# Kernel optimization log

Hardware: AMD Instinct MI355X
Metric: run time of the kernel (lower is better)

## Reference

```python
import jax, jax.numpy as jnp
import numpy as np

HEADS = 16
DIM_HEAD = 64

def setup_inputs() -> dict:
    key = jax.random.key(0)
    k1, k2, k3 = jax.random.split(key, 3)
    B, F, N, DIM = 4, 16, 196, 1024
    ntok = 1 + F * N  # cls + frames*patches
    x = jax.random.normal(k1, (B, ntok, DIM), dtype=jnp.float32)
    w_qkv = jax.random.normal(k2, (DIM, 3 * HEADS * DIM_HEAD), dtype=jnp.float32) * (DIM ** -0.5)
    w_out = jax.random.normal(k3, (HEADS * DIM_HEAD, DIM), dtype=jnp.float32) * ((HEADS * DIM_HEAD) ** -0.5)
    return {"x": x, "w_qkv": w_qkv, "w_out": w_out, "f": F}

def _attn(q, k, v):
    # q: [b, i, d], k/v: [b, j, d]
    sim = jnp.einsum('bid,bjd->bij', q, k)
    a = jax.nn.softmax(sim, axis=-1)
    return jnp.einsum('bij,bjd->bid', a, v)

def reference(x, w_qkv, w_out, f):
    B, ntok, dim = x.shape
    h, dh = HEADS, DIM_HEAD
    n = (ntok - 1) // f  # patches per frame
    scale = dh ** -0.5

    qkv = x @ w_qkv  # [B, ntok, 3*h*dh]
    q, k, v = jnp.split(qkv, 3, axis=-1)
    # 'b n (h d) -> (b h) n d'
    def split_heads(t):
        return t.reshape(B, ntok, h, dh).transpose(0, 2, 1, 3).reshape(B * h, ntok, dh)
    q, k, v = split_heads(q) * scale, split_heads(k), split_heads(v)

    cls_q, q_ = q[:, :1], q[:, 1:]
    cls_k, k_ = k[:, :1], k[:, 1:]
    cls_v, v_ = v[:, :1], v[:, 1:]

    # cls token attends to everything
    cls_out = _attn(cls_q, k, v)  # [(b h), 1, d]

    # axial rearrange: '(b h) (f n) d -> (b h f) n d' (spatial attention)
    def to_axial(t):
        return t.reshape(B * h, f, n, dh).reshape(B * h * f, n, dh)
    q_, k_, v_ = map(to_axial, (q_, k_, v_))

    # broadcast cls kv to each frame: 'b () d -> (b r) () d', r = f
    cls_k_r = jnp.repeat(cls_k, f, axis=0)
    cls_v_r = jnp.repeat(cls_v, f, axis=0)
    k_ = jnp.concatenate((cls_k_r, k_), axis=1)  # [(b h f), 1+n, d]
    v_ = jnp.concatenate((cls_v_r, v_), axis=1)

    out = _attn(q_, k_, v_)  # [(b h f), n, d]
    # back: '(b h f) n d -> (b h) (f n) d'
    out = out.reshape(B * h, f * n, dh)
    out = jnp.concatenate((cls_out, out), axis=1)  # [(b h), ntok, d]
    # '(b h) n d -> b n (h d)'
    out = out.reshape(B, h, ntok, dh).transpose(0, 2, 1, 3).reshape(B, ntok, h * dh)
    return out @ w_out
```

## Files before the change

### kernel.cpp

```cpp
#include <hip/hip_runtime.h>
#include <stdint.h>

typedef unsigned short u16;
typedef unsigned int u32;
typedef __attribute__((ext_vector_type(4))) float f32x4;
typedef __attribute__((ext_vector_type(4))) float float4v;
typedef __attribute__((ext_vector_type(8))) short short8;
typedef __attribute__((ext_vector_type(4))) u32 u32x4;
typedef __attribute__((ext_vector_type(4))) u16 u16x4;
typedef __attribute__((ext_vector_type(8))) u16 u16x8;

#define DEV static __device__ __forceinline__

#define NTOK 3137
#define MROWS 12548
#define NHEAD 16
#define DH 64
#define NKT 16

DEV float bf2f(u16 h){ u32 u = ((u32)h)<<16; float f; __builtin_memcpy(&f,&u,4); return f; }
DEV u16 f2bf(float f){ u32 u; __builtin_memcpy(&u,&f,4); u32 r = u + 0x7FFFu + ((u>>16)&1u); return (u16)(r>>16); }

DEV void gl_lds16(const u16* g, u16* l){
  __builtin_amdgcn_global_load_lds((const __attribute__((address_space(1))) void*)g,
                                   (__attribute__((address_space(3))) void*)l, 16, 0, 0);
}

#define BARRIER()  asm volatile("s_barrier" ::: "memory")
#define WAIT_LGKM0() asm volatile("s_waitcnt lgkmcnt(0)" ::: "memory")
#define WAIT_VM(n)  asm volatile("s_waitcnt vmcnt(" #n ")" ::: "memory")

__global__ __launch_bounds__(256) void cast_bf16_kernel(const float* __restrict__ in,
                                                        u16* __restrict__ out, int n4){
  int i = blockIdx.x*256 + threadIdx.x;
  int stride = gridDim.x*256;
  for(; i < n4; i += stride){
    float4v v = *(const float4v*)(in + (size_t)i*4);
    u16x4 o;
    for(int e=0;e<4;++e) o[e] = f2bf(v[e]);
    *(u16x4*)(out + (size_t)i*4) = o;
  }
}

__global__ void transpose_cast_kernel(const float* __restrict__ in, u16* __restrict__ out,
                                      int R, int C){
  __shared__ float tile[32][33];
  int c0 = blockIdx.x<<5, r0 = blockIdx.y<<5;
  int tx = threadIdx.x, ty = threadIdx.y;
  for(int k=0;k<32;k+=8) tile[ty+k][tx] = in[(size_t)(r0+ty+k)*C + c0+tx];
  __syncthreads();
  for(int k=0;k<32;k+=8) out[(size_t)(c0+ty+k)*R + r0+tx] = f2bf(tile[tx][ty+k]);
}

template<int EPI>
__global__ __launch_bounds__(512, 2) void gemm256_kernel(
    const u16* __restrict__ A, const u16* __restrict__ Bt,
    u16* __restrict__ Qb, u16* __restrict__ Kb, u16* __restrict__ Vb,
    float* __restrict__ Out, int Mtot, int tilesx)
{
  __shared__ __align__(16) char smem[131072];
  const int tid = threadIdx.x, lane = tid & 63, wid = tid >> 6;
  const int wr = wid >> 2, wc = wid & 3;

  const int nwg = gridDim.x, chunk = nwg >> 3, orig = blockIdx.x;
  const int wg = (orig & 7)*chunk + (orig >> 3);
  const int by = wg / tilesx, bx = wg - by*tilesx;
  const int m0 = by << 8, n0 = bx << 8;

  f32x4 acc[8][4];
  #pragma unroll
  for(int i=0;i<8;++i)
    #pragma unroll
    for(int j=0;j<4;++j) acc[i][j] = (f32x4){0.f,0.f,0.f,0.f};

  auto STAGE = [&](int t, int hi){
    const int bsel = t & 1;
    char* base = smem + bsel*65536 + ((hi>>1)<<15) + ((hi&1)<<14);
    const u16* mat = (hi < 2) ? A : Bt;
    const int rbase = ((hi < 2) ? m0 : n0) + ((hi&1)<<7);
    #pragma unroll
    for(int j=0;j<2;++j){
      int idx = j*512 + tid;
      int r = idx >> 3;
      int c2s = ((idx&7)<<4) ^ ((r&7)<<4);
      int grow = rbase + r;
      if(hi < 2 && grow >= Mtot) grow = Mtot - 1;
      const u16* src = mat + (size_t)grow*1024 + t*64 + (c2s>>1);
      u16* dst = (u16*)(base + j*8192 + wid*1024);
      gl_lds16(src, dst);
    }
  };

  const int rA   = (lane&15)*128;
  const int csw0 = (((lane>>4)<<4)      ) ^ ((lane&7)<<4);
  const int csw1 = (((lane>>4)<<4) + 64 ) ^ ((lane&7)<<4);

  auto RDA = [&](int bsel, int i, int kk)->short8 {
    const char* p = smem + bsel*65536 + (wr<<14) + (i<<4)*128 + rA + (kk ? csw1 : csw0);
    return *(const short8*)p;
  };
  auto RDB = [&](int bsel, int jn, int kk)->short8 {
    const char* p = smem + bsel*65536 + 32768 + ((wc>>1)<<14)
                  + (((wc&1)<<6) + (jn<<4))*128 + rA + (kk ? csw1 : csw0);
    return *(const short8*)p;
  };

  short8 aR[4][2], b0[2][2], b1[2][2];

  auto MFMA_Q = [&](int qi, int qj, short8 (&bv)[2][2]){
    #pragma unroll
    for(int i=0;i<4;++i)
      #pragma unroll
      for(int j=0;j<2;++j){
        acc[qi*4+i][qj*2+j] = __builtin_amdgcn_mfma_f32_16x16x32_bf16(aR[i][0], bv[j][0], acc[qi*4+i][qj*2+j], 0,0,0);
        acc[qi*4+i][qj*2+j] = __builtin_amdgcn_mfma_f32_16x16x32_bf16(aR[i][1], bv[j][1], acc[qi*4+i][qj*2+j], 0,0,0);
      }
  };

  auto DO_TILE = [&](int bs, int st1,int sh1, int st2,int sh2, int st3,int sh3, int st4,int sh4, bool lastv){
    #pragma unroll
    for(int i=0;i<4;++i){ aR[i][0]=RDA(bs,i,0); aR[i][1]=RDA(bs,i,1); }
    #pragma unroll
    for(int j=0;j<2;++j){ b0[j][0]=RDB(bs,j,0); b0[j][1]=RDB(bs,j,1); }
    if(st1 < NKT) STAGE(st1, sh1);
    asm volatile("s_waitcnt lgkmcnt(8)" ::: "memory");
    BARRIER(); WAIT_LGKM0();
    __builtin_amdgcn_s_setprio(1); MFMA_Q(0,0,b0); __builtin_amdgcn_s_setprio(0);
    BARRIER();
    #pragma unroll
    for(int j=0;j<2;++j){ b1[j][0]=RDB(bs,2+j,0); b1[j][1]=RDB(bs,2+j,1); }
    if(st2 < NKT) STAGE(st2, sh2);
    BARRIER(); WAIT_LGKM0();
    __builtin_amdgcn_s_setprio(1); MFMA_Q(0,1,b1); __builtin_amdgcn_s_setprio(0);
    BARRIER();
    #pragma unroll
    for(int i=0;i<4;++i){ aR[i][0]=RDA(bs,4+i,0); aR[i][1]=RDA(bs,4+i,1); }
    if(st3 < NKT) STAGE(st3, sh3);
    BARRIER(); WAIT_LGKM0();
    __builtin_amdgcn_s_setprio(1); MFMA_Q(1,1,b1); __builtin_amdgcn_s_setprio(0);
    BARRIER();
    if(st4 < NKT) STAGE(st4, sh4);
    BARRIER();
    __builtin_amdgcn_s_setprio(1); MFMA_Q(1,0,b0); __builtin_amdgcn_s_setprio(0);
    if(lastv){ WAIT_VM(0); } else { WAIT_VM(4); }
    BARRIER();
  };

  STAGE(0,2); STAGE(0,0); STAGE(0,3); STAGE(0,1); STAGE(1,2); STAGE(1,0);
  WAIT_VM(4);
  BARRIER();

  for(int u=0; u<NKT/2; ++u){
    const int tA = 2*u, tB = 2*u+1;
    const bool last = (u == NKT/2-1);
    DO_TILE(0, tB,3,   tB,1,   tA+2,2, tA+2,0, last);
    DO_TILE(1, tA+2,3, tA+2,1, tB+2,2, tB+2,0, last);
  }

  __syncthreads();

  if constexpr(EPI==0){
    const int which = n0 >> 10;
    const int hbase = (n0 & 1023) >> 6;
    const float sc = (which==0) ? 0.125f : 1.0f;
    u16* dst = (which==0)?Qb:((which==1)?Kb:Vb);
    u16* lC = (u16*)smem;
    for(int rh=0; rh<2; ++rh){
      if(wr == rh){
        #pragma unroll
        for(int i=0;i<8;++i){
          int rr = (i<<4) + ((lane>>4)<<2);
          #pragma unroll
          for(int j=0;j<4;++j){
            int ct = (wc<<6) + (j<<4) + (lane&15);
            #pragma unroll
            for(int r=0;r<4;++r) lC[(rr+r)*264 + ct] = f2bf(acc[i][j][r]*sc);
          }
        }
      }
      __syncthreads();
      for(int it=0; it<8; ++it){
        int idx = it*512 + tid;
        int row = idx >> 5, rest = idx & 31, hh = rest>>3, slot = rest&7;
        int mm = m0 + rh*128 + row;
        if(mm < Mtot){
          int b = mm / NTOK, tok = mm - b*NTOK;
          u16x8 v = *(const u16x8*)&lC[row*264 + hh*64 + slot*8];
          *(u16x8*)(dst + (((size_t)(b*NHEAD + hbase + hh)*NTOK + tok)<<6) + slot*8) = v;
        }
      }
      __syncthreads();
    }
  } else {
    float* lF = (float*)smem;
    for(int ph=0; ph<4; ++ph){
      int rh = ph>>1, ch = ph&1;
      if(wr==rh && (wc>>1)==ch){
        #pragma unroll
        for(int i=0;i<8;++i){
          int rr = (i<<4) + ((lane>>4)<<2);
          #pragma unroll
          for(int j=0;j<4;++j){
            int ct = ((wc&1)<<6) + (j<<4) + (lane&15);
            #pragma unroll
            for(int r=0;r<4;++r) lF[(rr+r)*132 + ct] = acc[i][j][r];
          }
        }
      }
      __syncthreads();
      for(int it=0; it<8; ++it){
        int idx = it*512 + tid;
        int row = idx >> 5, slot = idx & 31;
        int mm = m0 + rh*128 + row;
        if(mm < Mtot){
          float4v v = *(const float4v*)&lF[row*132 + slot*4];
          *(float4v*)(Out + (size_t)mm*1024 + n0 + ch*128 + slot*4) = v;
        }
      }
      __syncthreads();
    }
  }
}

__global__ __launch_bounds__(256) void cls_partial_kernel(
    const u16* __restrict__ Qb, const u16* __restrict__ Kb, const u16* __restrict__ Vb,
    float* __restrict__ part)
{
  __shared__ float qs[64];
  __shared__ float pbuf[4][64];
  __shared__ float wm[4], wl[4];
  __shared__ float wacc[4][64];
  const int tid = threadIdx.x, lane = tid & 63, wv = tid >> 6;
  const int c = blockIdx.x, bh = blockIdx.y;
  const u16* Kh = Kb + (size_t)bh*NTOK*DH;
  const u16* Vh = Vb + (size_t)bh*NTOK*DH;
  if(tid < 64) qs[tid] = bf2f(Qb[(size_t)bh*NTOK*DH + tid]);
  __syncthreads();

  const int jb = c*256 + wv*64;
  const int j = jb + lane;
  float s = -1e30f;
  if(j < NTOK){
    const u16* kr = Kh + (size_t)j*DH;
    float dot = 0.f;
    for(int t=0;t<8;++t){
      u16x8 kv = *(const u16x8*)(kr + t*8);
      for(int e=0;e<8;++e) dot += bf2f(kv[e]) * qs[t*8+e];
    }
    s = dot;
  }
  float mw = s;
  for(int off=1; off<64; off<<=1) mw = fmaxf(mw, __shfl_xor(mw, off));
  float p = (j < NTOK) ? __expf(s - mw) : 0.f;
  float lw = p;
  for(int off=1; off<64; off<<=1) lw += __shfl_xor(lw, off);
  pbuf[wv][lane] = p;

  float accd = 0.f;
  if(jb < NTOK){
    int nv = NTOK - jb; if(nv > 64) nv = 64;
    for(int jj=0; jj<nv; ++jj)
      accd += pbuf[wv][jj] * bf2f(Vh[(size_t)(jb+jj)*DH + lane]);
  }
  wacc[wv][lane] = accd;
  if(lane==0){ wm[wv]=mw; wl[wv]=lw; }
  __syncthreads();
  if(wv==0){
    float M = fmaxf(fmaxf(wm[0],wm[1]), fmaxf(wm[2],wm[3]));
    float L=0.f, Acc=0.f;
    for(int wi=0; wi<4; ++wi){
      float e = __expf(wm[wi]-M);
      L += wl[wi]*e; Acc += wacc[wi][lane]*e;
    }
    float* dstp = part + ((size_t)bh*13 + c)*68;
    if(lane==0){ dstp[0]=M; dstp[1]=L; }
    dstp[2+lane] = Acc;
  }
}

__global__ __launch_bounds__(64) void cls_reduce_kernel(
    const float* __restrict__ part, u16* __restrict__ Abuf)
{
  const int lane = threadIdx.x, bh = blockIdx.x;
  const float* p0 = part + (size_t)bh*13*68;
  float M = -1e30f;
  for(int i=0;i<13;++i) M = fmaxf(M, p0[i*68]);
  float L=0.f, Acc=0.f;
  for(int i=0;i<13;++i){
    float e = __expf(p0[i*68] - M);
    L += p0[i*68+1]*e;
    Acc += p0[i*68+2+lane]*e;
  }
  int b = bh>>4, h = bh&15;
  Abuf[(size_t)b*NTOK*1024 + h*DH + lane] = f2bf(Acc/L);
}

__global__ __launch_bounds__(256) void axial_attn_kernel(
    const u16* __restrict__ Qb, const u16* __restrict__ Kb, const u16* __restrict__ Vb,
    u16* __restrict__ Abuf)
{
  __shared__ u16 lV[64*232];
  __shared__ u16 lP[4*16*232];
  const int tid = threadIdx.x, lane = tid & 63, wv = tid >> 6;
  const int bf = blockIdx.x, bh = bf >> 4, fi = bf & 15;
  const u16* Kh = Kb + (size_t)bh*NTOK*DH;
  const u16* Vh = Vb + (size_t)bh*NTOK*DH;
  const u16* Qh = Qb + (size_t)bh*NTOK*DH;

  for(int c = tid; c < 224*8; c += 256){
    int tok = c >> 3, slot = c & 7;
    u16 vals[8];
    if(tok <= 196){
      size_t row = (tok==0) ? 0 : (size_t)(fi*196 + tok)*DH;
      u16x8 v = *(const u16x8*)(Vh + row + slot*8);
      for(int e=0;e<8;++e) vals[e] = v[e];
    } else {
      for(int e=0;e<8;++e) vals[e] = 0;
    }
    for(int e=0;e<8;++e) lV[(slot*8+e)*232 + tok] = vals[e];
  }
  for(int c = tid; c < 4*16*16; c += 256){
    int w2 = c >> 8, rem = c & 255, row = rem >> 4, cc = rem & 15;
    lP[w2*(16*232) + row*232 + 208 + cc] = 0;
  }
  __syncthreads();

  u16* myP = lP + wv*(16*232);
  const int b_i = bh >> 4, h = bh & 15;

  for(int qt = wv; qt < 13; qt += 4){
    int qr = qt*16 + (lane&15);
    int qrc = qr < 196 ? qr : 195;
    size_t qrow = (size_t)(1 + fi*196 + qrc)*DH;
    short8 qa0 = *(const short8*)(Qh + qrow + ((lane>>4)<<3));
    short8 qa1 = *(const short8*)(Qh + qrow + 32 + ((lane>>4)<<3));

    f32x4 s[13];
    for(int t=0;t<13;++t){
      int tok = t*16 + (lane&15);
      int tokc = tok < 197 ? tok : 196;
      size_t krow = (tokc==0) ? 0 : (size_t)(fi*196 + tokc)*DH;
      short8 b0v = *(const short8*)(Kh + krow + ((lane>>4)<<3));
      short8 b1v = *(const short8*)(Kh + krow + 32 + ((lane>>4)<<3));
      f32x4 z = {0.f,0.f,0.f,0.f};
      z = __builtin_amdgcn_mfma_f32_16x16x32_bf16(qa0, b0v, z, 0,0,0);
      z = __builtin_amdgcn_mfma_f32_16x16x32_bf16(qa1, b1v, z, 0,0,0);
      s[t] = z;
    }
    int mycol = lane & 15;
    if(192 + mycol >= 197)
      for(int r=0;r<4;++r) s[12][r] = -1e30f;

    f32x4 mx = s[0];
    for(int t=1;t<13;++t) for(int r=0;r<4;++r) mx[r] = fmaxf(mx[r], s[t][r]);
    for(int off=1; off<16; off<<=1)
      for(int r=0;r<4;++r) mx[r] = fmaxf(mx[r], __shfl_xor(mx[r], off));
    f32x4 lsum = {0.f,0.f,0.f,0.f};
    for(int t=0;t<13;++t) for(int r=0;r<4;++r){
      float p = __expf(s[t][r] - mx[r]); s[t][r] = p; lsum[r] += p;
    }
    for(int off=1; off<16; off<<=1)
      for(int r=0;r<4;++r) lsum[r] += __shfl_xor(lsum[r], off);

    for(int t=0;t<13;++t){
      int tok = t*16 + mycol;
      for(int r=0;r<4;++r) myP[(((lane>>4)<<2)+r)*232 + tok] = f2bf(s[t][r]);
    }

    f32x4 o[4] = {{0.f,0.f,0.f,0.f},{0.f,0.f,0.f,0.f},{0.f,0.f,0.f,0.f},{0.f,0.f,0.f,0.f}};
    for(int t2=0;t2<7;++t2){
      short8 a = *(const short8*)&myP[(lane&15)*232 + t2*32 + ((lane>>4)<<3)];
      for(int nd=0;nd<4;++nd){
        short8 b = *(const short8*)&lV[(nd*16 + (lane&15))*232 + t2*32 + ((lane>>4)<<3)];
        o[nd] = __builtin_amdgcn_mfma_f32_16x16x32_bf16(a, b, o[nd], 0,0,0);
      }
    }

    for(int nd=0; nd<4; ++nd){
      int d = nd*16 + (lane&15);
      for(int r=0;r<4;++r){
        int rr = ((lane>>4)<<2) + r;
        myP[rr*72 + d] = f2bf(o[nd][r] / lsum[r]);
      }
    }
    asm volatile("s_waitcnt lgkmcnt(0)" ::: "memory");
    for(int it=0; it<2; ++it){
      int idx = it*64 + lane;
      int row = idx >> 3, slot = idx & 7;
      int ql = qt*16 + row;
      if(ql < 196){
        u16x8 v = *(const u16x8*)&myP[row*72 + slot*8];
        int tok = 1 + fi*196 + ql;
        *(u16x8*)(Abuf + ((size_t)b_i*NTOK + tok)*1024 + h*DH + slot*8) = v;
      }
    }
  }
}

extern "C" void kernel_launch(void* const* d_in, const int* in_sizes, int n_in,
                              void* d_out, int out_size, void* d_ws, size_t ws_size,
                              hipStream_t stream) {
  const float* x     = (const float*)d_in[0];
  const float* wqkv  = (const float*)d_in[1];
  const float* wout  = (const float*)d_in[2];
  float* out = (float*)d_out;
  char* ws = (char*)d_ws;

  u16* xb     = (u16*)(ws);
  u16* Abuf   = xb;
  u16* wqkvT  = (u16*)(ws + 25698304);
  float* clsPart = (float*)(ws + 25698304);
  u16* woutT  = (u16*)(ws + 31989760);
  u16* Qb     = (u16*)(ws + 34086912);
  u16* Kb     = (u16*)(ws + 59785216);
  u16* Vb     = (u16*)(ws + 85483520);

  cast_bf16_kernel<<<dim3(2048), dim3(256), 0, stream>>>(x, xb, (MROWS*1024)/4);
  transpose_cast_kernel<<<dim3(96,32), dim3(32,8), 0, stream>>>(wqkv, wqkvT, 1024, 3072);
  transpose_cast_kernel<<<dim3(32,32), dim3(32,8), 0, stream>>>(wout, woutT, 1024, 1024);

  gemm256_kernel<0><<<dim3(600), dim3(512), 0, stream>>>(xb, wqkvT, Qb, Kb, Vb, nullptr, MROWS, 12);

  cls_partial_kernel<<<dim3(13,64), dim3(256), 0, stream>>>(Qb, Kb, Vb, clsPart);
  cls_reduce_kernel<<<dim3(64), dim3(64), 0, stream>>>(clsPart, Abuf);
  axial_attn_kernel<<<dim3(1024), dim3(256), 0, stream>>>(Qb, Kb, Vb, Abuf);

  gemm256_kernel<1><<<dim3(200), dim3(512), 0, stream>>>(Abuf, woutT, nullptr, nullptr, nullptr, out, MROWS, 4);
}
```

Before: 212.8 us.

## Merge prep kernels, fuse cls and axial attention, restructure GEMM LDS staging

Folds the cast and two transpose-cast kernels into one prep launch, and merges the cls-partial and axial attention kernels into one launch that dispatches on block index. It also restructures the GEMM main loop to stage K-halves of 32 columns with a new paired-row swizzled LDS layout, issuing all 8x4 MFMAs per phase from freshly loaded fragments. The aim is fewer launches and better load/compute overlap in the GEMM. The new swizzle and wait counts carry correctness and bank-conflict risk.

```diff
diff --git a/kernel.cpp b/kernel.cpp
--- a/kernel.cpp
+++ b/kernel.cpp
@@ -30,26 +30,35 @@
 #define WAIT_LGKM0() asm volatile("s_waitcnt lgkmcnt(0)" ::: "memory")
 #define WAIT_VM(n)  asm volatile("s_waitcnt vmcnt(" #n ")" ::: "memory")
 
-__global__ __launch_bounds__(256) void cast_bf16_kernel(const float* __restrict__ in,
-                                                        u16* __restrict__ out, int n4){
-  int i = blockIdx.x*256 + threadIdx.x;
-  int stride = gridDim.x*256;
-  for(; i < n4; i += stride){
-    float4v v = *(const float4v*)(in + (size_t)i*4);
-    u16x4 o;
-    for(int e=0;e<4;++e) o[e] = f2bf(v[e]);
-    *(u16x4*)(out + (size_t)i*4) = o;
-  }
-}
-
-__global__ void transpose_cast_kernel(const float* __restrict__ in, u16* __restrict__ out,
-                                      int R, int C){
+__global__ __launch_bounds__(256) void prep_kernel(
+    const float* __restrict__ x, const float* __restrict__ wqkv, const float* __restrict__ wout,
+    u16* __restrict__ xb, u16* __restrict__ wqkvT, u16* __restrict__ woutT)
+{
   __shared__ float tile[32][33];
-  int c0 = blockIdx.x<<5, r0 = blockIdx.y<<5;
-  int tx = threadIdx.x, ty = threadIdx.y;
-  for(int k=0;k<32;k+=8) tile[ty+k][tx] = in[(size_t)(r0+ty+k)*C + c0+tx];
-  __syncthreads();
-  for(int k=0;k<32;k+=8) out[(size_t)(c0+ty+k)*R + r0+tx] = f2bf(tile[tx][ty+k]);
+  const int bid = blockIdx.x, tid = threadIdx.x;
+  if(bid < 2048){
+    const int n4 = (MROWS*1024)/4;
+    for(int i = bid*256 + tid; i < n4; i += 2048*256){
+      float4v v = *(const float4v*)(x + (size_t)i*4);
+      u16x4 o;
+      for(int e=0;e<4;++e) o[e] = f2bf(v[e]);
+      *(u16x4*)(xb + (size_t)i*4) = o;
+    }
+  } else {
+    const float* in; u16* out; int C, c0, r0;
+    if(bid < 2048+3072){
+      int tb = bid - 2048; in = wqkv; out = wqkvT; C = 3072;
+      c0 = (tb%96)<<5; r0 = (tb/96)<<5;
+    } else {
+      int tb = bid - 5120; in = wout; out = woutT; C = 1024;
+      c0 = (tb&31)<<5; r0 = (tb>>5)<<5;
+    }
+    const int R = 1024;
+    int tx = tid&31, ty = tid>>5;
+    for(int k=0;k<32;k+=8) tile[ty+k][tx] = in[(size_t)(r0+ty+k)*C + c0+tx];
+    __syncthreads();
+    for(int k=0;k<32;k+=8) out[(size_t)(c0+ty+k)*R + r0+tx] = f2bf(tile[tx][ty+k]);
+  }
 }
 
 template<int EPI>
@@ -73,89 +82,65 @@
     #pragma unroll
     for(int j=0;j<4;++j) acc[i][j] = (f32x4){0.f,0.f,0.f,0.f};
 
-  auto STAGE = [&](int t, int hi){
+  auto STAGE = [&](int t, int kh){
     const int bsel = t & 1;
-    char* base = smem + bsel*65536 + ((hi>>1)<<15) + ((hi&1)<<14);
-    const u16* mat = (hi < 2) ? A : Bt;
-    const int rbase = ((hi < 2) ? m0 : n0) + ((hi&1)<<7);
+    char* rbase = smem + bsel*65536 + kh*32768;
     #pragma unroll
-    for(int j=0;j<2;++j){
-      int idx = j*512 + tid;
-      int r = idx >> 3;
-      int c2s = ((idx&7)<<4) ^ ((r&7)<<4);
-      int grow = rbase + r;
-      if(hi < 2 && grow >= Mtot) grow = Mtot - 1;
-      const u16* src = mat + (size_t)grow*1024 + t*64 + (c2s>>1);
-      u16* dst = (u16*)(base + j*8192 + wid*1024);
+    for(int c=0;c<4;++c){
+      const int half = c & 1;
+      const int isB  = c >> 1;
+      int slotpos = (half<<9) + tid;
+      int pair = slotpos >> 3;
+      int sl   = (slotpos & 7) ^ (pair & 7);
+      int grow = (isB ? n0 : m0) + pair*2 + (sl>>2);
+      if(!isB && grow >= Mtot) grow = Mtot - 1;
+      const u16* src = (isB ? Bt : A) + (size_t)grow*1024 + t*64 + kh*32 + (sl&3)*8;
+      u16* dst = (u16*)(rbase + (isB<<14) + (half<<13) + wid*1024);
       gl_lds16(src, dst);
     }
   };
 
-  const int rA   = (lane&15)*128;
-  const int csw0 = (((lane>>4)<<4)      ) ^ ((lane&7)<<4);
-  const int csw1 = (((lane>>4)<<4) + 64 ) ^ ((lane&7)<<4);
-
-  auto RDA = [&](int bsel, int i, int kk)->short8 {
-    const char* p = smem + bsel*65536 + (wr<<14) + (i<<4)*128 + rA + (kk ? csw1 : csw0);
-    return *(const short8*)p;
-  };
-  auto RDB = [&](int bsel, int jn, int kk)->short8 {
-    const char* p = smem + bsel*65536 + 32768 + ((wc>>1)<<14)
-                  + (((wc&1)<<6) + (jn<<4))*128 + rA + (kk ? csw1 : csw0);
-    return *(const short8*)p;
-  };
-
-  short8 aR[4][2], b0[2][2], b1[2][2];
-
-  auto MFMA_Q = [&](int qi, int qj, short8 (&bv)[2][2]){
+  const int pl = (lane&15)>>1;
+  const int sprime = ((((lane&1)<<2) | (lane>>4)) ^ pl);
+  const int laneoff = pl*128 + sprime*16;
+
+  auto PHASE = [&](int bsel, int t, int kh, int stT, int stKh, int vmode){
+    short8 af[8], bfv[4];
+    const char* rb = smem + bsel*65536 + kh*32768;
     #pragma unroll
-    for(int i=0;i<4;++i)
+    for(int i=0;i<8;++i) af[i]  = *(const short8*)(rb + (wr<<13) + (i<<10) + laneoff);
+    #pragma unroll
+    for(int j=0;j<4;++j) bfv[j] = *(const short8*)(rb + 16384 + (wc<<12) + (j<<10) + laneoff);
+    if(stT < NKT) STAGE(stT, stKh);
+    asm volatile("s_waitcnt lgkmcnt(8)" ::: "memory");
+    BARRIER();
+    WAIT_LGKM0();
+    __builtin_amdgcn_s_setprio(1);
+    #pragma unroll
+    for(int i=0;i<8;++i)
       #pragma unroll
-      for(int j=0;j<2;++j){
-        acc[qi*4+i][qj*2+j] = __builtin_amdgcn_mfma_f32_16x16x32_bf16(aR[i][0], bv[j][0], acc[qi*4+i][qj*2+j], 0,0,0);
-        acc[qi*4+i][qj*2+j] = __builtin_amdgcn_mfma_f32_16x16x32_bf16(aR[i][1], bv[j][1], acc[qi*4+i][qj*2+j], 0,0,0);
-      }
-  };
-
-  auto DO_TILE = [&](int bs, int st1,int sh1, int st2,int sh2, int st3,int sh3, int st4,int sh4, bool lastv){
-    #pragma unroll
-    for(int i=0;i<4;++i){ aR[i][0]=RDA(bs,i,0); aR[i][1]=RDA(bs,i,1); }
-    #pragma unroll
-    for(int j=0;j<2;++j){ b0[j][0]=RDB(bs,j,0); b0[j][1]=RDB(bs,j,1); }
-    if(st1 < NKT) STAGE(st1, sh1);
-    asm volatile("s_waitcnt lgkmcnt(8)" ::: "memory");
-    BARRIER(); WAIT_LGKM0();
-    __builtin_amdgcn_s_setprio(1); MFMA_Q(0,0,b0); __builtin_amdgcn_s_setprio(0);
-    BARRIER();
-    #pragma unroll
-    for(int j=0;j<2;++j){ b1[j][0]=RDB(bs,2+j,0); b1[j][1]=RDB(bs,2+j,1); }
-    if(st2 < NKT) STAGE(st2, sh2);
-    BARRIER(); WAIT_LGKM0();
-    __builtin_amdgcn_s_setprio(1); MFMA_Q(0,1,b1); __builtin_amdgcn_s_setprio(0);
-    BARRIER();
-    #pragma unroll
-    for(int i=0;i<4;++i){ aR[i][0]=RDA(bs,4+i,0); aR[i][1]=RDA(bs,4+i,1); }
-    if(st3 < NKT) STAGE(st3, sh3);
-    BARRIER(); WAIT_LGKM0();
-    __builtin_amdgcn_s_setprio(1); MFMA_Q(1,1,b1); __builtin_amdgcn_s_setprio(0);
-    BARRIER();
-    if(st4 < NKT) STAGE(st4, sh4);
-    BARRIER();
-    __builtin_amdgcn_s_setprio(1); MFMA_Q(1,0,b0); __builtin_amdgcn_s_setprio(0);
-    if(lastv){ WAIT_VM(0); } else { WAIT_VM(4); }
+      for(int j=0;j<4;++j)
+        acc[i][j] = __builtin_amdgcn_mfma_f32_16x16x32_bf16(af[i], bfv[j], acc[i][j], 0,0,0);
+    __builtin_amdgcn_s_setprio(0);
+    if(vmode==0){ WAIT_VM(8); } else if(vmode==1){ WAIT_VM(4); } else { WAIT_VM(0); }
     BARRIER();
   };
 
-  STAGE(0,2); STAGE(0,0); STAGE(0,3); STAGE(0,1); STAGE(1,2); STAGE(1,0);
-  WAIT_VM(4);
+  STAGE(0,0); STAGE(0,1); STAGE(1,0);
+  WAIT_VM(8);
   BARRIER();
 
-  for(int u=0; u<NKT/2; ++u){
+  for(int u=0; u<7; ++u){
     const int tA = 2*u, tB = 2*u+1;
-    const bool last = (u == NKT/2-1);
-    DO_TILE(0, tB,3,   tB,1,   tA+2,2, tA+2,0, last);
-    DO_TILE(1, tA+2,3, tA+2,1, tB+2,2, tB+2,0, last);
-  }
+    PHASE(0, tA, 0, tA+1, 1, 0);
+    PHASE(0, tA, 1, tA+2, 0, 0);
+    PHASE(1, tB, 0, tB+1, 1, 0);
+    PHASE(1, tB, 1, tB+2, 0, 0);
+  }
+  PHASE(0, 14, 0, 15, 1, 0);
+  PHASE(0, 14, 1, 16, 0, 1);
+  PHASE(1, 15, 0, 16, 1, 2);
+  PHASE(1, 15, 1, 16, 0, 2);
 
   __syncthreads();
 
@@ -222,59 +207,160 @@
   }
 }
 
-__global__ __launch_bounds__(256) void cls_partial_kernel(
+__global__ __launch_bounds__(256) void attn_kernel(
     const u16* __restrict__ Qb, const u16* __restrict__ Kb, const u16* __restrict__ Vb,
-    float* __restrict__ part)
+    float* __restrict__ part, u16* __restrict__ Abuf)
 {
+  __shared__ u16 lV[64*232];
+  __shared__ u16 lP[4*16*232];
   __shared__ float qs[64];
   __shared__ float pbuf[4][64];
-  __shared__ float wm[4], wl[4];
+  __shared__ float wmx[4], wls[4];
   __shared__ float wacc[4][64];
   const int tid = threadIdx.x, lane = tid & 63, wv = tid >> 6;
-  const int c = blockIdx.x, bh = blockIdx.y;
+
+  if(blockIdx.x >= 1024){
+    const int idx = blockIdx.x - 1024;
+    const int c = idx >> 6, bh = idx & 63;
+    const u16* Kh = Kb + (size_t)bh*NTOK*DH;
+    const u16* Vh = Vb + (size_t)bh*NTOK*DH;
+    if(tid < 64) qs[tid] = bf2f(Qb[(size_t)bh*NTOK*DH + tid]);
+    __syncthreads();
+
+    const int jb = c*256 + wv*64;
+    const int j = jb + lane;
+    float s = -1e30f;
+    if(j < NTOK){
+      const u16* kr = Kh + (size_t)j*DH;
+      float dot = 0.f;
+      for(int t=0;t<8;++t){
+        u16x8 kv = *(const u16x8*)(kr + t*8);
+        for(int e=0;e<8;++e) dot += bf2f(kv[e]) * qs[t*8+e];
+      }
+      s = dot;
+    }
+    float mw = s;
+    for(int off=1; off<64; off<<=1) mw = fmaxf(mw, __shfl_xor(mw, off));
+    float p = (j < NTOK) ? __expf(s - mw) : 0.f;
+    float lw = p;
+    for(int off=1; off<64; off<<=1) lw += __shfl_xor(lw, off);
+    pbuf[wv][lane] = p;
+
+    float accd = 0.f;
+    if(jb < NTOK){
+      int nv = NTOK - jb; if(nv > 64) nv = 64;
+      for(int jj=0; jj<nv; ++jj)
+        accd += pbuf[wv][jj] * bf2f(Vh[(size_t)(jb+jj)*DH + lane]);
+    }
+    wacc[wv][lane] = accd;
+    if(lane==0){ wmx[wv]=mw; wls[wv]=lw; }
+    __syncthreads();
+    if(wv==0){
+      float M = fmaxf(fmaxf(wmx[0],wmx[1]), fmaxf(wmx[2],wmx[3]));
+      float L=0.f, Acc=0.f;
+      for(int wi=0; wi<4; ++wi){
+        float e = __expf(wmx[wi]-M);
+        L += wls[wi]*e; Acc += wacc[wi][lane]*e;
+      }
+      float* dstp = part + ((size_t)bh*13 + c)*68;
+      if(lane==0){ dstp[0]=M; dstp[1]=L; }
+      dstp[2+lane] = Acc;
+    }
+    return;
+  }
+
+  const int bf = blockIdx.x, bh = bf >> 4, fi = bf & 15;
   const u16* Kh = Kb + (size_t)bh*NTOK*DH;
   const u16* Vh = Vb + (size_t)bh*NTOK*DH;
-  if(tid < 64) qs[tid] = bf2f(Qb[(size_t)bh*NTOK*DH + tid]);
+  const u16* Qh = Qb + (size_t)bh*NTOK*DH;
+
+  for(int c = tid; c < 224*8; c += 256){
+    int tok = c >> 3, slot = c & 7;
+    u16 vals[8];
+    if(tok <= 196){
+      size_t row = (tok==0) ? 0 : (size_t)(fi*196 + tok)*DH;
+      u16x8 v = *(const u16x8*)(Vh + row + slot*8);
+      for(int e=0;e<8;++e) vals[e] = v[e];
+    } else {
+      for(int e=0;e<8;++e) vals[e] = 0;
+    }
+    for(int e=0;e<8;++e) lV[(slot*8+e)*232 + tok] = vals[e];
+  }
+  for(int c = tid; c < 4*16*16; c += 256){
+    int w2 = c >> 8, rem = c & 255, row = rem >> 4, cc = rem & 15;
+    lP[w2*(16*232) + row*232 + 208 + cc] = 0;
+  }
   __syncthreads();
 
-  const int jb = c*256 + wv*64;
-  const int j = jb + lane;
-  float s = -1e30f;
-  if(j < NTOK){
-    const u16* kr = Kh + (size_t)j*DH;
-    float dot = 0.f;
-    for(int t=0;t<8;++t){
-      u16x8 kv = *(const u16x8*)(kr + t*8);
-      for(int e=0;e<8;++e) dot += bf2f(kv[e]) * qs[t*8+e];
-    }
-    s = dot;
-  }
-  float mw = s;
-  for(int off=1; off<64; off<<=1) mw = fmaxf(mw, __shfl_xor(mw, off));
-  float p = (j < NTOK) ? __expf(s - mw) : 0.f;
-  float lw = p;
-  for(int off=1; off<64; off<<=1) lw += __shfl_xor(lw, off);
-  pbuf[wv][lane] = p;
-
-  float accd = 0.f;
-  if(jb < NTOK){
-    int nv = NTOK - jb; if(nv > 64) nv = 64;
-    for(int jj=0; jj<nv; ++jj)
-      accd += pbuf[wv][jj] * bf2f(Vh[(size_t)(jb+jj)*DH + lane]);
-  }
-  wacc[wv][lane] = accd;
-  if(lane==0){ wm[wv]=mw; wl[wv]=lw; }
-  __syncthreads();
-  if(wv==0){
-    float M = fmaxf(fmaxf(wm[0],wm[1]), fmaxf(wm[2],wm[3]));
-    float L=0.f, Acc=0.f;
-    for(int wi=0; wi<4; ++wi){
-      float e = __expf(wm[wi]-M);
-      L += wl[wi]*e; Acc += wacc[wi][lane]*e;
-    }
-    float* dstp = part + ((size_t)bh*13 + c)*68;
-    if(lane==0){ dstp[0]=M; dstp[1]=L; }
-    dstp[2+lane] = Acc;
+  u16* myP = lP + wv*(16*232);
+  const int b_i = bh >> 4, h = bh & 15;
+
+  for(int qt = wv; qt < 13; qt += 4){
+    int qr = qt*16 + (lane&15);
+    int qrc = qr < 196 ? qr : 195;
+    size_t qrow = (size_t)(1 + fi*196 + qrc)*DH;
+    short8 qa0 = *(const short8*)(Qh + qrow + ((lane>>4)<<3));
+    short8 qa1 = *(const short8*)(Qh + qrow + 32 + ((lane>>4)<<3));
+
+    f32x4 s[13];
+    for(int t=0;t<13;++t){
+      int tok = t*16 + (lane&15);
+      int tokc = tok < 197 ? tok : 196;
+      size_t krow = (tokc==0) ? 0 : (size_t)(fi*196 + tokc)*DH;
+      short8 b0v = *(const short8*)(Kh + krow + ((lane>>4)<<3));
+      short8 b1v = *(const short8*)(Kh + krow + 32 + ((lane>>4)<<3));
+      f32x4 z = {0.f,0.f,0.f,0.f};
+      z = __builtin_amdgcn_mfma_f32_16x16x32_bf16(qa0, b0v, z, 0,0,0);
+      z = __builtin_amdgcn_mfma_f32_16x16x32_bf16(qa1, b1v, z, 0,0,0);
+      s[t] = z;
+    }
+    int mycol = lane & 15;
+    if(192 + mycol >= 197)
+      for(int r=0;r<4;++r) s[12][r] = -1e30f;
+
+    f32x4 mx = s[0];
+    for(int t=1;t<13;++t) for(int r=0;r<4;++r) mx[r] = fmaxf(mx[r], s[t][r]);
+    for(int off=1; off<16; off<<=1)
+      for(int r=0;r<4;++r) mx[r] = fmaxf(mx[r], __shfl_xor(mx[r], off));
+    f32x4 lsum = {0.f,0.f,0.f,0.f};
+    for(int t=0;t<13;++t) for(int r=0;r<4;++r){
+      float p = __expf(s[t][r] - mx[r]); s[t][r] = p; lsum[r] += p;
+    }
+    for(int off=1; off<16; off<<=1)
+      for(int r=0;r<4;++r) lsum[r] += __shfl_xor(lsum[r], off);
+
+    for(int t=0;t<13;++t){
+      int tok = t*16 + mycol;
+      for(int r=0;r<4;++r) myP[(((lane>>4)<<2)+r)*232 + tok] = f2bf(s[t][r]);
+    }
+
+    f32x4 o[4] = {{0.f,0.f,0.f,0.f},{0.f,0.f,0.f,0.f},{0.f,0.f,0.f,0.f},{0.f,0.f,0.f,0.f}};
+    for(int t2=0;t2<7;++t2){
+      short8 a = *(const short8*)&myP[(lane&15)*232 + t2*32 + ((lane>>4)<<3)];
+      for(int nd=0;nd<4;++nd){
+        short8 b = *(const short8*)&lV[(nd*16 + (lane&15))*232 + t2*32 + ((lane>>4)<<3)];
+        o[nd] = __builtin_amdgcn_mfma_f32_16x16x32_bf16(a, b, o[nd], 0,0,0);
+      }
+    }
+
+    for(int nd=0; nd<4; ++nd){
+      int d = nd*16 + (lane&15);
+      for(int r=0;r<4;++r){
+        int rr = ((lane>>4)<<2) + r;
+        myP[rr*72 + d] = f2bf(o[nd][r] / lsum[r]);
+      }
+    }
+    asm volatile("s_waitcnt lgkmcnt(0)" ::: "memory");
+    for(int it=0; it<2; ++it){
+      int idx = it*64 + lane;
+      int row = idx >> 3, slot = idx & 7;
+      int ql = qt*16 + row;
+      if(ql < 196){
+        u16x8 v = *(const u16x8*)&myP[row*72 + slot*8];
+        int tok = 1 + fi*196 + ql;
+        *(u16x8*)(Abuf + ((size_t)b_i*NTOK + tok)*1024 + h*DH + slot*8) = v;
+      }
+    }
   }
 }
 
@@ -295,108 +381,6 @@
   Abuf[(size_t)b*NTOK*1024 + h*DH + lane] = f2bf(Acc/L);
 }
 
-__global__ __launch_bounds__(256) void axial_attn_kernel(
-    const u16* __restrict__ Qb, const u16* __restrict__ Kb, const u16* __restrict__ Vb,
-    u16* __restrict__ Abuf)
-{
-  __shared__ u16 lV[64*232];
-  __shared__ u16 lP[4*16*232];
-  const int tid = threadIdx.x, lane = tid & 63, wv = tid >> 6;
-  const int bf = blockIdx.x, bh = bf >> 4, fi = bf & 15;
-  const u16* Kh = Kb + (size_t)bh*NTOK*DH;
-  const u16* Vh = Vb + (size_t)bh*NTOK*DH;
-  const u16* Qh = Qb + (size_t)bh*NTOK*DH;
-
-  for(int c = tid; c < 224*8; c += 256){
-    int tok = c >> 3, slot = c & 7;
-    u16 vals[8];
-    if(tok <= 196){
-      size_t row = (tok==0) ? 0 : (size_t)(fi*196 + tok)*DH;
-      u16x8 v = *(const u16x8*)(Vh + row + slot*8);
-      for(int e=0;e<8;++e) vals[e] = v[e];
-    } else {
-      for(int e=0;e<8;++e) vals[e] = 0;
-    }
-    for(int e=0;e<8;++e) lV[(slot*8+e)*232 + tok] = vals[e];
-  }
-  for(int c = tid; c < 4*16*16; c += 256){
-    int w2 = c >> 8, rem = c & 255, row = rem >> 4, cc = rem & 15;
-    lP[w2*(16*232) + row*232 + 208 + cc] = 0;
-  }
-  __syncthreads();
-
-  u16* myP = lP + wv*(16*232);
-  const int b_i = bh >> 4, h = bh & 15;
-
-  for(int qt = wv; qt < 13; qt += 4){
-    int qr = qt*16 + (lane&15);
-    int qrc = qr < 196 ? qr : 195;
-    size_t qrow = (size_t)(1 + fi*196 + qrc)*DH;
-    short8 qa0 = *(const short8*)(Qh + qrow + ((lane>>4)<<3));
-    short8 qa1 = *(const short8*)(Qh + qrow + 32 + ((lane>>4)<<3));
-
-    f32x4 s[13];
-    for(int t=0;t<13;++t){
-      int tok = t*16 + (lane&15);
-      int tokc = tok < 197 ? tok : 196;
-      size_t krow = (tokc==0) ? 0 : (size_t)(fi*196 + tokc)*DH;
-      short8 b0v = *(const short8*)(Kh + krow + ((lane>>4)<<3));
-      short8 b1v = *(const short8*)(Kh + krow + 32 + ((lane>>4)<<3));
-      f32x4 z = {0.f,0.f,0.f,0.f};
-      z = __builtin_amdgcn_mfma_f32_16x16x32_bf16(qa0, b0v, z, 0,0,0);
-      z = __builtin_amdgcn_mfma_f32_16x16x32_bf16(qa1, b1v, z, 0,0,0);
-      s[t] = z;
-    }
-    int mycol = lane & 15;
-    if(192 + mycol >= 197)
-      for(int r=0;r<4;++r) s[12][r] = -1e30f;
-
-    f32x4 mx = s[0];
-    for(int t=1;t<13;++t) for(int r=0;r<4;++r) mx[r] = fmaxf(mx[r], s[t][r]);
-    for(int off=1; off<16; off<<=1)
-      for(int r=0;r<4;++r) mx[r] = fmaxf(mx[r], __shfl_xor(mx[r], off));
-    f32x4 lsum = {0.f,0.f,0.f,0.f};
-    for(int t=0;t<13;++t) for(int r=0;r<4;++r){
-      float p = __expf(s[t][r] - mx[r]); s[t][r] = p; lsum[r] += p;
-    }
-    for(int off=1; off<16; off<<=1)
-      for(int r=0;r<4;++r) lsum[r] += __shfl_xor(lsum[r], off);
-
-    for(int t=0;t<13;++t){
-      int tok = t*16 + mycol;
-      for(int r=0;r<4;++r) myP[(((lane>>4)<<2)+r)*232 + tok] = f2bf(s[t][r]);
-    }
-
-    f32x4 o[4] = {{0.f,0.f,0.f,0.f},{0.f,0.f,0.f,0.f},{0.f,0.f,0.f,0.f},{0.f,0.f,0.f,0.f}};
-    for(int t2=0;t2<7;++t2){
-      short8 a = *(const short8*)&myP[(lane&15)*232 + t2*32 + ((lane>>4)<<3)];
-      for(int nd=0;nd<4;++nd){
-        short8 b = *(const short8*)&lV[(nd*16 + (lane&15))*232 + t2*32 + ((lane>>4)<<3)];
-        o[nd] = __builtin_amdgcn_mfma_f32_16x16x32_bf16(a, b, o[nd], 0,0,0);
-      }
-    }
-
-    for(int nd=0; nd<4; ++nd){
-      int d = nd*16 + (lane&15);
-      for(int r=0;r<4;++r){
-        int rr = ((lane>>4)<<2) + r;
-        myP[rr*72 + d] = f2bf(o[nd][r] / lsum[r]);
-      }
-    }
-    asm volatile("s_waitcnt lgkmcnt(0)" ::: "memory");
-    for(int it=0; it<2; ++it){
-      int idx = it*64 + lane;
-      int row = idx >> 3, slot = idx & 7;
-      int ql = qt*16 + row;
-      if(ql < 196){
-        u16x8 v = *(const u16x8*)&myP[row*72 + slot*8];
-        int tok = 1 + fi*196 + ql;
-        *(u16x8*)(Abuf + ((size_t)b_i*NTOK + tok)*1024 + h*DH + slot*8) = v;
-      }
-    }
-  }
-}
-
 extern "C" void kernel_launch(void* const* d_in, const int* in_sizes, int n_in,
                               void* d_out, int out_size, void* d_ws, size_t ws_size,
                               hipStream_t stream) {
@@ -415,15 +399,12 @@
   u16* Kb     = (u16*)(ws + 59785216);
   u16* Vb     = (u16*)(ws + 85483520);
 
-  cast_bf16_kernel<<<dim3(2048), dim3(256), 0, stream>>>(x, xb, (MROWS*1024)/4);
-  transpose_cast_kernel<<<dim3(96,32), dim3(32,8), 0, stream>>>(wqkv, wqkvT, 1024, 3072);
-  transpose_cast_kernel<<<dim3(32,32), dim3(32,8), 0, stream>>>(wout, woutT, 1024, 1024);
+  prep_kernel<<<dim3(6144), dim3(256), 0, stream>>>(x, wqkv, wout, xb, wqkvT, woutT);
 
   gemm256_kernel<0><<<dim3(600), dim3(512), 0, stream>>>(xb, wqkvT, Qb, Kb, Vb, nullptr, MROWS, 12);
 
-  cls_partial_kernel<<<dim3(13,64), dim3(256), 0, stream>>>(Qb, Kb, Vb, clsPart);
+  attn_kernel<<<dim3(1856), dim3(256), 0, stream>>>(Qb, Kb, Vb, clsPart, Abuf);
   cls_reduce_kernel<<<dim3(64), dim3(64), 0, stream>>>(clsPart, Abuf);
-  axial_attn_kernel<<<dim3(1024), dim3(256), 0, stream>>>(Qb, Kb, Vb, Abuf);
 
   gemm256_kernel<1><<<dim3(200), dim3(512), 0, stream>>>(Abuf, woutT, nullptr, nullptr, nullptr, out, MROWS, 4);
 }
```

New measurement: 206.5 us. -2.9%, faster.
